# Performance work log

Hardware: AMD Instinct MI355X
Metric: run time of the kernel (lower is better)

The kernel has to match this reference:

```python
import jax, jax.numpy as jnp
import numpy as np
from jax import lax

B, CIN, COUT, H, W = 4, 256, 256, 64, 64
KH = KW = 3
K = KH * KW
GN_GROUPS = 32
EPS = 1e-5


def setup_inputs() -> dict:
    key = jax.random.key(0)
    ks = jax.random.split(key, 6)
    x = jax.random.normal(ks[0], (B, CIN, H, W), jnp.float32)
    # offset predictor conv: 3x3, 18 out channels, with bias (init small so offsets stay near 0)
    offset_w = jax.random.normal(ks[1], (2 * K, CIN, KH, KW), jnp.float32) * 0.01
    offset_b = jax.random.normal(ks[2], (2 * K,), jnp.float32) * 0.01
    # deformable conv weight (no bias), He-ish scale
    deform_w = jax.random.normal(ks[3], (COUT, CIN, KH, KW), jnp.float32) * (1.0 / np.sqrt(CIN * K))
    gn_gamma = jnp.ones((COUT,), jnp.float32)
    gn_beta = jnp.zeros((COUT,), jnp.float32)
    return {"x": x, "offset_w": offset_w, "offset_b": offset_b,
            "deform_w": deform_w, "gn_gamma": gn_gamma, "gn_beta": gn_beta}


def _deform_conv(x, offset, weight):
    """Deformable conv v1, stride=1, pad=1, dil=1, deformable_groups=1.
    x: [B,C,H,W]; offset: [B,2K,H,W] with (dy,dx) per kernel tap; weight: [O,C,3,3].
    """
    b, c, h, w = x.shape
    off = offset.reshape(b, K, 2, h, w)
    # base sampling grid per kernel tap: p = p0 - pad + k
    ky, kx = jnp.meshgrid(jnp.arange(KH), jnp.arange(KW), indexing="ij")
    base_y = (jnp.arange(h, dtype=jnp.float32) - 1.0)[None, :, None] + ky.reshape(K).astype(jnp.float32)[:, None, None]  # [K,H,1]
    base_x = (jnp.arange(w, dtype=jnp.float32) - 1.0)[None, None, :] + kx.reshape(K).astype(jnp.float32)[:, None, None]  # [K,1,W]
    py = base_y[None] + off[:, :, 0]  # [B,K,H,W]
    px = base_x[None] + off[:, :, 1]  # [B,K,H,W]

    y0 = jnp.floor(py)
    x0 = jnp.floor(px)
    ty = py - y0
    tx = px - x0
    y0 = y0.astype(jnp.int32)
    x0 = x0.astype(jnp.int32)

    x_hw = x.transpose(0, 2, 3, 1).reshape(b, h * w, c)  # [B,HW,C]

    def corner(yi, xi, wgt):
        valid = (yi >= 0) & (yi < h) & (xi >= 0) & (xi < w)
        yc = jnp.clip(yi, 0, h - 1)
        xc = jnp.clip(xi, 0, w - 1)
        idx = (yc * w + xc).reshape(b, K * h * w)
        v = jnp.take_along_axis(x_hw, idx[..., None], axis=1)  # [B,KHW,C]
        return v * (wgt * valid.astype(wgt.dtype)).reshape(b, K * h * w, 1)

    samp = (corner(y0, x0, (1 - ty) * (1 - tx))
            + corner(y0, x0 + 1, (1 - ty) * tx)
            + corner(y0 + 1, x0, ty * (1 - tx))
            + corner(y0 + 1, x0 + 1, ty * tx))  # [B,KHW,C]
    samp = samp.reshape(b, K, h, w, c)
    return jnp.einsum("bkhwc,ock->bohw", samp, weight.reshape(weight.shape[0], c, K))


def reference(x, offset_w, offset_b, deform_w, gn_gamma, gn_beta):
    # offset = conv3x3(x) + bias
    offset = lax.conv_general_dilated(
        x, offset_w, window_strides=(1, 1), padding=((1, 1), (1, 1)),
        dimension_numbers=("NCHW", "OIHW", "NCHW")) + offset_b[None, :, None, None]
    out = _deform_conv(x, offset, deform_w)
    # GroupNorm(32, COUT) + ReLU
    b, c, h, w = out.shape
    g = out.reshape(b, GN_GROUPS, (c // GN_GROUPS) * h * w)
    mu = g.mean(axis=2, keepdims=True)
    var = g.var(axis=2, keepdims=True)
    g = (g - mu) * lax.rsqrt(var + EPS)
    out = g.reshape(b, c, h, w) * gn_gamma[None, :, None, None] + gn_beta[None, :, None, None]
    return jax.nn.relu(out)
```

## Files before the change

kernel.cpp:

```cpp
#include <hip/hip_runtime.h>
#include <hip/hip_bf16.h>
#include <stdint.h>


typedef unsigned short u16;
typedef __bf16 bf16x8 __attribute__((ext_vector_type(8)));
typedef float f32x4_t __attribute__((ext_vector_type(4)));

#define HW 4096

__device__ __forceinline__ uint32_t f32_to_bf16_rne(float f) {
  uint32_t u = __builtin_bit_cast(uint32_t, f);
  return (u + 0x7FFFu + ((u >> 16) & 1u)) >> 16;
}
__device__ __forceinline__ float bf_lo(uint32_t u) {
  return __builtin_bit_cast(float, u << 16);
}
__device__ __forceinline__ float bf_hi(uint32_t u) {
  return __builtin_bit_cast(float, u & 0xFFFF0000u);
}
__device__ __forceinline__ uint32_t blend2(uint32_t a, uint32_t b, uint32_t c,
                                           uint32_t d, float4 mw) {
  float lo = mw.x * bf_lo(a) + mw.y * bf_lo(b) + mw.z * bf_lo(c) + mw.w * bf_lo(d);
  float hi = mw.x * bf_hi(a) + mw.y * bf_hi(b) + mw.z * bf_hi(c) + mw.w * bf_hi(d);
  return f32_to_bf16_rne(lo) | (f32_to_bf16_rne(hi) << 16);
}

__global__ __launch_bounds__(256) void k_pre(const float* __restrict__ x,
                                             const float* __restrict__ wsrc,
                                             const float* __restrict__ ow,
                                             u16* __restrict__ xt,
                                             u16* __restrict__ warr,
                                             u16* __restrict__ owm,
                                             float* __restrict__ part) {
  __shared__ float tile[64][65];
  int bid = blockIdx.x;
  int tid = threadIdx.x;
  int bz = bid >> 8;
  int c0 = ((bid >> 6) & 3) * 64;
  int p0 = (bid & 63) * 64;

  {
    int ch = tid >> 4;
    int q4 = (tid & 15) * 4;
#pragma unroll
    for (int r = 0; r < 4; r++) {
      int c = r * 16 + ch;
      float4 v = *(const float4*)&x[((size_t)(bz * 256 + c0 + c)) * HW + p0 + q4];
      tile[c][q4 + 0] = v.x;
      tile[c][q4 + 1] = v.y;
      tile[c][q4 + 2] = v.z;
      tile[c][q4 + 3] = v.w;
    }
  }
  __syncthreads();
  {
    int chunk = tid & 7;
    int pxr = tid >> 3;
#pragma unroll
    for (int it = 0; it < 2; it++) {
      int px = it * 32 + pxr;
      int cb = chunk * 8;
      uint4 u;
      u.x = f32_to_bf16_rne(tile[cb + 0][px]) | (f32_to_bf16_rne(tile[cb + 1][px]) << 16);
      u.y = f32_to_bf16_rne(tile[cb + 2][px]) | (f32_to_bf16_rne(tile[cb + 3][px]) << 16);
      u.z = f32_to_bf16_rne(tile[cb + 4][px]) | (f32_to_bf16_rne(tile[cb + 5][px]) << 16);
      u.w = f32_to_bf16_rne(tile[cb + 6][px]) | (f32_to_bf16_rne(tile[cb + 7][px]) << 16);
      *(uint4*)&xt[((size_t)(bz * HW + p0 + px)) * 256 + c0 + cb] = u;
    }
  }

#pragma unroll
  for (int k = 0; k < 3; k++) {
    int i = k * 256 + tid;
    if (i < 576) {
      int e = bid * 576 + i;
      int kk = e & 7, m = (e >> 3) & 255, g = (e >> 11) & 7, kc = e >> 14;
      int cin = (kc & 3) * 64 + g * 8 + kk;
      warr[e] = (u16)f32_to_bf16_rne(wsrc[m * 2304 + cin * 9 + (kc >> 2)]);
    }
  }
  if (tid < 72) {
    int e = bid * 72 + tid;
    int kk = e & 7, m = (e >> 3) & 31, g = (e >> 8) & 7, kc = e >> 11;
    int cin = (kc & 3) * 64 + g * 8 + kk;
    float v = (m < 18) ? ow[m * 2304 + cin * 9 + (kc >> 2)] : 0.f;
    owm[e] = (u16)f32_to_bf16_rne(v);
  }
  if (bid == 0 && tid < 256) part[tid] = 0.f;
}

__global__ __launch_bounds__(512, 4) void k_conv(
    const u16* __restrict__ xt, const u16* __restrict__ warr,
    const u16* __restrict__ owm, const float* __restrict__ ob,
    float* __restrict__ out, float* __restrict__ part) {
  __shared__ char smem[54272];
  u16* stage = (u16*)smem;
  float* off_part = (float*)(smem + 33792);
  int4* ci_s = (int4*)smem;
  float4* mw_s = (float4*)(smem + 4608);
  u16* b_s = (u16*)(smem + 9216);

  int tid = threadIdx.x;
  int lane = tid & 63;
  int wm = tid >> 6;
  int wk = (blockIdx.x & 7) * 64 + (blockIdx.x >> 3);
  int b = wk >> 7;
  int pt = wk & 127;
  int p0 = pt * 32;
  int yrow = p0 >> 6, xbase = p0 & 63;

  {
    u16* st = stage + wm * 2112;
    int q = lane & 15, pq = lane >> 4;
    int oct = lane & 7, pxs = lane >> 3;
    f32x4_t a2[2][2] = {};
#pragma unroll 1
    for (int kc = wm; kc < 36; kc += 8) {
      int tap = kc >> 2, cc = kc & 3;
      int ky = tap / 3, kx = tap % 3;
      int yy = yrow + ky - 1;
      bool vy = (yy >= 0) && (yy < 64);
#pragma unroll
      for (int i = 0; i < 4; i++) {
        int px = i * 8 + pxs;
        int xx2 = xbase + px + kx - 1;
        uint4 v = make_uint4(0u, 0u, 0u, 0u);
        if (vy && xx2 >= 0 && xx2 < 64)
          v = *(const uint4*)&xt[(b * HW + yy * 64 + xx2) * 256 + cc * 64 + oct * 8];
        *(uint4*)&st[oct * 264 + px * 8] = v;
      }
#pragma unroll
      for (int ks = 0; ks < 2; ks++) {
        int g = ks * 4 + pq;
        const u16* ab = owm + kc * 2048 + g * 256;
#pragma unroll
        for (int s = 0; s < 2; s++) {
          bf16x8 bfr = *(bf16x8*)&st[g * 264 + (s * 16 + q) * 8];
#pragma unroll
          for (int im = 0; im < 2; im++) {
            bf16x8 af = *(const bf16x8*)&ab[(im * 16 + q) * 8];
            a2[s][im] = __builtin_amdgcn_mfma_f32_16x16x32_bf16(af, bfr, a2[s][im], 0, 0, 0);
          }
        }
      }
    }
#pragma unroll
    for (int s = 0; s < 2; s++)
#pragma unroll
      for (int im = 0; im < 2; im++)
#pragma unroll
        for (int r = 0; r < 4; r++) {
          int oc = im * 16 + pq * 4 + r;
          if (oc < 18) off_part[(wm * 32 + s * 16 + q) * 20 + oc] = a2[s][im][r];
        }
  }
  __syncthreads();
  for (int it = tid; it < 288; it += 512) {
    int tap = it >> 5;
    int px = it & 31;
    float dy = ob[2 * tap], dx = ob[2 * tap + 1];
#pragma unroll
    for (int wv = 0; wv < 8; wv++) {
      dy += off_part[(wv * 32 + px) * 20 + 2 * tap];
      dx += off_part[(wv * 32 + px) * 20 + 2 * tap + 1];
    }
    int ky = tap / 3, kx = tap % 3;
    int p = p0 + px;
    int yq = p >> 6, xq = p & 63;
    float py = (float)(yq - 1 + ky) + dy;
    float pxx = (float)(xq - 1 + kx) + dx;
    float y0f = floorf(py), x0f = floorf(pxx);
    float ty = py - y0f, tx = pxx - x0f;
    int y0 = (int)y0f, x0 = (int)x0f;
    int y1 = y0 + 1, x1 = x0 + 1;
    float wy0 = 1.f - ty, wy1 = ty, wx0 = 1.f - tx, wx1 = tx;
    bool vy0 = (y0 >= 0) && (y0 < 64), vy1 = (y1 >= 0) && (y1 < 64);
    bool vx0 = (x0 >= 0) && (x0 < 64), vx1 = (x1 >= 0) && (x1 < 64);
    int cy0 = min(max(y0, 0), 63), cy1 = min(max(y1, 0), 63);
    int cx0 = min(max(x0, 0), 63), cx1 = min(max(x1, 0), 63);
    int base = b * HW;
    int4 ci;
    ci.x = (base + cy0 * 64 + cx0) * 256;
    ci.y = (base + cy0 * 64 + cx1) * 256;
    ci.z = (base + cy1 * 64 + cx0) * 256;
    ci.w = (base + cy1 * 64 + cx1) * 256;
    float4 mw;
    mw.x = wy0 * wx0 * ((vy0 && vx0) ? 1.f : 0.f);
    mw.y = wy0 * wx1 * ((vy0 && vx1) ? 1.f : 0.f);
    mw.z = wy1 * wx0 * ((vy1 && vx0) ? 1.f : 0.f);
    mw.w = wy1 * wx1 * ((vy1 && vx1) ? 1.f : 0.f);
    ci_s[it] = ci;
    mw_s[it] = mw;
  }
  __syncthreads();

  {
    int oct8 = tid & 15;
    int pxg = tid >> 4;
    int sub = pxg >> 4;
    int pxw = pxg & 15;
    int col = lane & 15;
    int pq = lane >> 4;
    int e0 = oct8 * 8;
    f32x4_t acc[2][2] = {};

    int4 ci = ci_s[pxg];
    float4 mw = mw_s[pxg];
    uint4 A0 = *(const uint4*)&xt[ci.x + e0];
    uint4 A1 = *(const uint4*)&xt[ci.y + e0];
    uint4 A2 = *(const uint4*)&xt[ci.z + e0];
    uint4 A3 = *(const uint4*)&xt[ci.w + e0];
    uint4 G0 = *(const uint4*)&xt[ci.x + 128 + e0];
    uint4 G1 = *(const uint4*)&xt[ci.y + 128 + e0];
    uint4 G2 = *(const uint4*)&xt[ci.z + 128 + e0];
    uint4 G3 = *(const uint4*)&xt[ci.w + 128 + e0];

#pragma unroll 1
    for (int dp = 0; dp < 9; dp++) {
      u16* bb = b_s + (dp & 1) * 8704;
      {
        uint4 u;
        u.x = blend2(A0.x, A1.x, A2.x, A3.x, mw);
        u.y = blend2(A0.y, A1.y, A2.y, A3.y, mw);
        u.z = blend2(A0.z, A1.z, A2.z, A3.z, mw);
        u.w = blend2(A0.w, A1.w, A2.w, A3.w, mw);
        *(uint4*)&bb[sub * 2176 + oct8 * 136 + pxw * 8] = u;
      }
      {
        uint4 v;
        v.x = blend2(G0.x, G1.x, G2.x, G3.x, mw);
        v.y = blend2(G0.y, G1.y, G2.y, G3.y, mw);
        v.z = blend2(G0.z, G1.z, G2.z, G3.z, mw);
        v.w = blend2(G0.w, G1.w, G2.w, G3.w, mw);
        *(uint4*)&bb[4352 + sub * 2176 + oct8 * 136 + pxw * 8] = v;
      }
      __syncthreads();
      if (dp < 8) {
        ci = ci_s[(dp + 1) * 32 + pxg];
        float4 mwn = mw_s[(dp + 1) * 32 + pxg];
        A0 = *(const uint4*)&xt[ci.x + e0];
        A1 = *(const uint4*)&xt[ci.y + e0];
        A2 = *(const uint4*)&xt[ci.z + e0];
        A3 = *(const uint4*)&xt[ci.w + e0];
        G0 = *(const uint4*)&xt[ci.x + 128 + e0];
        G1 = *(const uint4*)&xt[ci.y + 128 + e0];
        G2 = *(const uint4*)&xt[ci.z + 128 + e0];
        G3 = *(const uint4*)&xt[ci.w + 128 + e0];
        mw = mwn;
      }
      __builtin_amdgcn_s_setprio(1);
#pragma unroll
      for (int ks = 0; ks < 8; ks++) {
        int set = ks >> 2;
        int ro = (ks & 3) * 4 + pq;
        const u16* bp = bb + set * 4352 + ro * 136 + col * 8;
        bf16x8 bb0 = *(const bf16x8*)&bp[0];
        bf16x8 bb1 = *(const bf16x8*)&bp[2176];
        int kc = dp * 4 + (ks >> 1);
        int gg = (ks & 1) * 4 + pq;
        const u16* ab = warr + kc * 16384 + gg * 2048 + (wm * 32 + col) * 8;
#pragma unroll
        for (int im = 0; im < 2; im++) {
          bf16x8 af = *(const bf16x8*)&ab[im * 128];
          acc[0][im] = __builtin_amdgcn_mfma_f32_16x16x32_bf16(af, bb0, acc[0][im], 0, 0, 0);
          acc[1][im] = __builtin_amdgcn_mfma_f32_16x16x32_bf16(af, bb1, acc[1][im], 0, 0, 0);
        }
      }
      __builtin_amdgcn_s_setprio(0);
    }

#pragma unroll
    for (int im = 0; im < 2; im++) {
      float s = 0.f, ss = 0.f;
#pragma unroll
      for (int sb = 0; sb < 2; sb++) {
        int n = p0 + sb * 16 + col;
#pragma unroll
        for (int r = 0; r < 4; r++) {
          int m = wm * 32 + im * 16 + pq * 4 + r;
          float v = acc[sb][im][r];
          out[(b * 256 + m) * HW + n] = v;
          s += v;
          ss += v * v;
        }
      }
#pragma unroll
      for (int msk = 1; msk <= 16; msk <<= 1) {
        s += __shfl_xor(s, msk);
        ss += __shfl_xor(ss, msk);
      }
      if ((lane & 31) == 0) {
        int grp = wm * 4 + im * 2 + (lane >> 5);
        float* pp = part + (b * 32 + grp) * 2;
        atomicAdd(pp, s);
        atomicAdd(pp + 1, ss);
      }
    }
  }
}

__global__ __launch_bounds__(256) void k_gn_apply(float* __restrict__ out,
                                                  const float2* __restrict__ part,
                                                  const float* __restrict__ gamma,
                                                  const float* __restrict__ beta) {
  int base = blockIdx.x * 512 + threadIdx.x;
#pragma unroll
  for (int k = 0; k < 2; k++) {
    int gid = base + k * 256;
    int c = (gid >> 10) & 255;
    int bb = gid >> 18;
    float2 p = part[bb * 32 + (c >> 3)];
    float mu = p.x / 32768.f;
    float var = p.y / 32768.f - mu * mu;
    float rs = rsqrtf(var + 1e-5f);
    float ga = gamma[c] * rs;
    float be = beta[c] - mu * ga;
    float4 v = ((const float4*)out)[gid];
    v.x = fmaxf(v.x * ga + be, 0.f);
    v.y = fmaxf(v.y * ga + be, 0.f);
    v.z = fmaxf(v.z * ga + be, 0.f);
    v.w = fmaxf(v.w * ga + be, 0.f);
    ((float4*)out)[gid] = v;
  }
}

extern "C" void kernel_launch(void* const* d_in, const int* in_sizes, int n_in,
                              void* d_out, int out_size, void* d_ws, size_t ws_size,
                              hipStream_t stream) {
  const float* x = (const float*)d_in[0];
  const float* offset_w = (const float*)d_in[1];
  const float* offset_b = (const float*)d_in[2];
  const float* deform_w = (const float*)d_in[3];
  const float* gn_gamma = (const float*)d_in[4];
  const float* gn_beta = (const float*)d_in[5];
  float* out = (float*)d_out;
  char* ws = (char*)d_ws;

  u16* xt = (u16*)ws;
  u16* warr = (u16*)(ws + 8388608);
  u16* owm = (u16*)(ws + 9568256);
  float* part = (float*)(ws + 9715712);

  k_pre<<<dim3(1024), dim3(256), 0, stream>>>(x, deform_w, offset_w, xt, warr, owm, part);
  k_conv<<<dim3(512), dim3(512), 0, stream>>>(xt, warr, owm, offset_b, out, part);
  k_gn_apply<<<dim3(2048), dim3(256), 0, stream>>>(out, (const float2*)part, gn_gamma, gn_beta);
}
```

Measured before the change: 158.6 us.

## Fuse GroupNorm apply into conv kernel via per-batch grid barrier

Removes the separate GroupNorm/ReLU kernel. Each conv block now adds its partial statistics, signals a per-batch atomic counter, spins until all 128 blocks of that batch have arrived, then normalizes and applies ReLU to its accumulators before writing the output once. This drops the extra read and write of the full output tensor and one kernel launch. In exchange it relies on all 128 blocks of a batch being co-resident, since the spin barrier would deadlock otherwise, and blocks sit idle while they wait.

```diff
diff --git a/kernel.cpp b/kernel.cpp
--- a/kernel.cpp
+++ b/kernel.cpp
@@ -87,13 +87,17 @@
     float v = (m < 18) ? ow[m * 2304 + cin * 9 + (kc >> 2)] : 0.f;
     owm[e] = (u16)f32_to_bf16_rne(v);
   }
-  if (bid == 0 && tid < 256) part[tid] = 0.f;
+  if (bid == 0) {
+    if (tid < 256) part[tid] = 0.f;
+    if (tid < 4) ((int*)(part + 256))[tid] = 0;
+  }
 }
 
 __global__ __launch_bounds__(512, 4) void k_conv(
     const u16* __restrict__ xt, const u16* __restrict__ warr,
     const u16* __restrict__ owm, const float* __restrict__ ob,
-    float* __restrict__ out, float* __restrict__ part) {
+    const float* __restrict__ gamma, const float* __restrict__ beta,
+    float* __restrict__ out, float* __restrict__ part, int* __restrict__ cnt) {
   __shared__ char smem[54272];
   u16* stage = (u16*)smem;
   float* off_part = (float*)(smem + 33792);
@@ -195,15 +199,15 @@
   }
   __syncthreads();
 
+  int col = lane & 15;
+  int pq = lane >> 4;
+  f32x4_t acc[2][2] = {};
   {
     int oct8 = tid & 15;
     int pxg = tid >> 4;
     int sub = pxg >> 4;
     int pxw = pxg & 15;
-    int col = lane & 15;
-    int pq = lane >> 4;
     int e0 = oct8 * 8;
-    f32x4_t acc[2][2] = {};
 
     int4 ci = ci_s[pxg];
     float4 mw = mw_s[pxg];
@@ -269,59 +273,71 @@
       }
       __builtin_amdgcn_s_setprio(0);
     }
-
-#pragma unroll
-    for (int im = 0; im < 2; im++) {
-      float s = 0.f, ss = 0.f;
+  }
+
+#pragma unroll
+  for (int im = 0; im < 2; im++) {
+    float s = 0.f, ss = 0.f;
+#pragma unroll
+    for (int sb = 0; sb < 2; sb++)
+#pragma unroll
+      for (int r = 0; r < 4; r++) {
+        float v = acc[sb][im][r];
+        s += v;
+        ss += v * v;
+      }
+#pragma unroll
+    for (int msk = 1; msk <= 16; msk <<= 1) {
+      s += __shfl_xor(s, msk);
+      ss += __shfl_xor(ss, msk);
+    }
+    if ((lane & 31) == 0) {
+      int grp = wm * 4 + im * 2 + (lane >> 5);
+      float* pp = part + (b * 32 + grp) * 2;
+      atomicAdd(pp, s);
+      atomicAdd(pp + 1, ss);
+    }
+  }
+
+  __threadfence();
+  __syncthreads();
+  if (tid == 0) {
+    __hip_atomic_fetch_add(&cnt[b], 1, __ATOMIC_ACQ_REL, __HIP_MEMORY_SCOPE_AGENT);
+    while (__hip_atomic_load(&cnt[b], __ATOMIC_ACQUIRE, __HIP_MEMORY_SCOPE_AGENT) < 128) {
+      __builtin_amdgcn_s_sleep(2);
+    }
+  }
+  __syncthreads();
+
+  float* gmu = (float*)smem;
+  float* grs = (float*)(smem + 128);
+  if (tid < 32) {
+    float s = __hip_atomic_load(&part[(b * 32 + tid) * 2], __ATOMIC_RELAXED,
+                                __HIP_MEMORY_SCOPE_AGENT);
+    float ss = __hip_atomic_load(&part[(b * 32 + tid) * 2 + 1], __ATOMIC_RELAXED,
+                                 __HIP_MEMORY_SCOPE_AGENT);
+    float mu = s * (1.f / 32768.f);
+    float var = ss * (1.f / 32768.f) - mu * mu;
+    gmu[tid] = mu;
+    grs[tid] = rsqrtf(var + 1e-5f);
+  }
+  __syncthreads();
+
+#pragma unroll
+  for (int im = 0; im < 2; im++) {
+    int grp = wm * 4 + im * 2 + (lane >> 5);
+    float mu = gmu[grp], rs = grs[grp];
+#pragma unroll
+    for (int r = 0; r < 4; r++) {
+      int m = wm * 32 + im * 16 + pq * 4 + r;
+      float ga = gamma[m] * rs;
+      float be = beta[m] - mu * ga;
 #pragma unroll
       for (int sb = 0; sb < 2; sb++) {
         int n = p0 + sb * 16 + col;
-#pragma unroll
-        for (int r = 0; r < 4; r++) {
-          int m = wm * 32 + im * 16 + pq * 4 + r;
-          float v = acc[sb][im][r];
-          out[(b * 256 + m) * HW + n] = v;
-          s += v;
-          ss += v * v;
-        }
-      }
-#pragma unroll
-      for (int msk = 1; msk <= 16; msk <<= 1) {
-        s += __shfl_xor(s, msk);
-        ss += __shfl_xor(ss, msk);
-      }
-      if ((lane & 31) == 0) {
-        int grp = wm * 4 + im * 2 + (lane >> 5);
-        float* pp = part + (b * 32 + grp) * 2;
-        atomicAdd(pp, s);
-        atomicAdd(pp + 1, ss);
-      }
-    }
-  }
-}
-
-__global__ __launch_bounds__(256) void k_gn_apply(float* __restrict__ out,
-                                                  const float2* __restrict__ part,
-                                                  const float* __restrict__ gamma,
-                                                  const float* __restrict__ beta) {
-  int base = blockIdx.x * 512 + threadIdx.x;
-#pragma unroll
-  for (int k = 0; k < 2; k++) {
-    int gid = base + k * 256;
-    int c = (gid >> 10) & 255;
-    int bb = gid >> 18;
-    float2 p = part[bb * 32 + (c >> 3)];
-    float mu = p.x / 32768.f;
-    float var = p.y / 32768.f - mu * mu;
-    float rs = rsqrtf(var + 1e-5f);
-    float ga = gamma[c] * rs;
-    float be = beta[c] - mu * ga;
-    float4 v = ((const float4*)out)[gid];
-    v.x = fmaxf(v.x * ga + be, 0.f);
-    v.y = fmaxf(v.y * ga + be, 0.f);
-    v.z = fmaxf(v.z * ga + be, 0.f);
-    v.w = fmaxf(v.w * ga + be, 0.f);
-    ((float4*)out)[gid] = v;
+        out[(b * 256 + m) * HW + n] = fmaxf(acc[sb][im][r] * ga + be, 0.f);
+      }
+    }
   }
 }
 
@@ -341,8 +357,9 @@
   u16* warr = (u16*)(ws + 8388608);
   u16* owm = (u16*)(ws + 9568256);
   float* part = (float*)(ws + 9715712);
+  int* cnt = (int*)(ws + 9715712 + 1024);
 
   k_pre<<<dim3(1024), dim3(256), 0, stream>>>(x, deform_w, offset_w, xt, warr, owm, part);
-  k_conv<<<dim3(512), dim3(512), 0, stream>>>(xt, warr, owm, offset_b, out, part);
-  k_gn_apply<<<dim3(2048), dim3(256), 0, stream>>>(out, (const float2*)part, gn_gamma, gn_beta);
-}
+  k_conv<<<dim3(512), dim3(512), 0, stream>>>(xt, warr, owm, offset_b, gn_gamma,
+                                              gn_beta, out, part, cnt);
+}
```

New measurement: 215.3 us. +35.8%, slower.

## Halve conv block pixel tile to 16 with 4 waves each covering 64 channels

Applied to the files above, without the earlier changes.

The fused deformable-conv kernel now handles 16 pixels per block with 256 threads instead of 32 pixels with 512 threads, doubling the grid to 1024 blocks. Each wave now computes 64 output channels against one 16-pixel B fragment, so four MFMAs share each B load. The offset-predictor conv is redistributed over 4 waves by tap. Shared memory drops from about 54KB to 22KB, which should allow more resident blocks and spread the work more evenly. The cost is that each weight fragment is reused across fewer pixels, so global weight reads per output roughly double, and per-block setup overhead is repeated more often.

```diff
diff --git a/kernel.cpp b/kernel.cpp
--- a/kernel.cpp
+++ b/kernel.cpp
@@ -90,80 +90,78 @@
   if (bid == 0 && tid < 256) part[tid] = 0.f;
 }
 
-__global__ __launch_bounds__(512, 4) void k_conv(
+__global__ __launch_bounds__(256, 4) void k_conv(
     const u16* __restrict__ xt, const u16* __restrict__ warr,
     const u16* __restrict__ owm, const float* __restrict__ ob,
     float* __restrict__ out, float* __restrict__ part) {
-  __shared__ char smem[54272];
+  __shared__ char smem[22016];
   u16* stage = (u16*)smem;
-  float* off_part = (float*)(smem + 33792);
+  float* off_part = (float*)(smem + 8704);
   int4* ci_s = (int4*)smem;
-  float4* mw_s = (float4*)(smem + 4608);
-  u16* b_s = (u16*)(smem + 9216);
+  float4* mw_s = (float4*)(smem + 2304);
+  u16* b_s = (u16*)(smem + 4608);
 
   int tid = threadIdx.x;
   int lane = tid & 63;
   int wm = tid >> 6;
-  int wk = (blockIdx.x & 7) * 64 + (blockIdx.x >> 3);
-  int b = wk >> 7;
-  int pt = wk & 127;
-  int p0 = pt * 32;
+  int wk = (blockIdx.x & 7) * 128 + (blockIdx.x >> 3);
+  int b = wk >> 8;
+  int pt = wk & 255;
+  int p0 = pt * 16;
   int yrow = p0 >> 6, xbase = p0 & 63;
 
   {
-    u16* st = stage + wm * 2112;
+    u16* st = stage + wm * 1088;
     int q = lane & 15, pq = lane >> 4;
     int oct = lane & 7, pxs = lane >> 3;
-    f32x4_t a2[2][2] = {};
+    f32x4_t a2[2] = {};
 #pragma unroll 1
-    for (int kc = wm; kc < 36; kc += 8) {
-      int tap = kc >> 2, cc = kc & 3;
+    for (int tap = wm; tap < 9; tap += 4) {
       int ky = tap / 3, kx = tap % 3;
       int yy = yrow + ky - 1;
       bool vy = (yy >= 0) && (yy < 64);
 #pragma unroll
-      for (int i = 0; i < 4; i++) {
-        int px = i * 8 + pxs;
-        int xx2 = xbase + px + kx - 1;
-        uint4 v = make_uint4(0u, 0u, 0u, 0u);
-        if (vy && xx2 >= 0 && xx2 < 64)
-          v = *(const uint4*)&xt[(b * HW + yy * 64 + xx2) * 256 + cc * 64 + oct * 8];
-        *(uint4*)&st[oct * 264 + px * 8] = v;
-      }
-#pragma unroll
-      for (int ks = 0; ks < 2; ks++) {
-        int g = ks * 4 + pq;
-        const u16* ab = owm + kc * 2048 + g * 256;
-#pragma unroll
-        for (int s = 0; s < 2; s++) {
-          bf16x8 bfr = *(bf16x8*)&st[g * 264 + (s * 16 + q) * 8];
+      for (int cc = 0; cc < 4; cc++) {
+        int kc = tap * 4 + cc;
+#pragma unroll
+        for (int i = 0; i < 2; i++) {
+          int px = i * 8 + pxs;
+          int xx2 = xbase + px + kx - 1;
+          uint4 v = make_uint4(0u, 0u, 0u, 0u);
+          if (vy && xx2 >= 0 && xx2 < 64)
+            v = *(const uint4*)&xt[(b * HW + yy * 64 + xx2) * 256 + cc * 64 + oct * 8];
+          *(uint4*)&st[oct * 136 + px * 8] = v;
+        }
+#pragma unroll
+        for (int ks = 0; ks < 2; ks++) {
+          int g = ks * 4 + pq;
+          const u16* ab = owm + kc * 2048 + g * 256;
+          bf16x8 bfr = *(bf16x8*)&st[g * 136 + q * 8];
 #pragma unroll
           for (int im = 0; im < 2; im++) {
             bf16x8 af = *(const bf16x8*)&ab[(im * 16 + q) * 8];
-            a2[s][im] = __builtin_amdgcn_mfma_f32_16x16x32_bf16(af, bfr, a2[s][im], 0, 0, 0);
+            a2[im] = __builtin_amdgcn_mfma_f32_16x16x32_bf16(af, bfr, a2[im], 0, 0, 0);
           }
         }
       }
     }
 #pragma unroll
-    for (int s = 0; s < 2; s++)
-#pragma unroll
-      for (int im = 0; im < 2; im++)
-#pragma unroll
-        for (int r = 0; r < 4; r++) {
-          int oc = im * 16 + pq * 4 + r;
-          if (oc < 18) off_part[(wm * 32 + s * 16 + q) * 20 + oc] = a2[s][im][r];
-        }
+    for (int im = 0; im < 2; im++)
+#pragma unroll
+      for (int r = 0; r < 4; r++) {
+        int oc = im * 16 + pq * 4 + r;
+        if (oc < 18) off_part[(wm * 16 + q) * 20 + oc] = a2[im][r];
+      }
   }
   __syncthreads();
-  for (int it = tid; it < 288; it += 512) {
-    int tap = it >> 5;
-    int px = it & 31;
+  if (tid < 144) {
+    int tap = tid >> 4;
+    int px = tid & 15;
     float dy = ob[2 * tap], dx = ob[2 * tap + 1];
 #pragma unroll
-    for (int wv = 0; wv < 8; wv++) {
-      dy += off_part[(wv * 32 + px) * 20 + 2 * tap];
-      dx += off_part[(wv * 32 + px) * 20 + 2 * tap + 1];
+    for (int wv = 0; wv < 4; wv++) {
+      dy += off_part[(wv * 16 + px) * 20 + 2 * tap];
+      dx += off_part[(wv * 16 + px) * 20 + 2 * tap + 1];
     }
     int ky = tap / 3, kx = tap % 3;
     int p = p0 + px;
@@ -190,20 +188,18 @@
     mw.y = wy0 * wx1 * ((vy0 && vx1) ? 1.f : 0.f);
     mw.z = wy1 * wx0 * ((vy1 && vx0) ? 1.f : 0.f);
     mw.w = wy1 * wx1 * ((vy1 && vx1) ? 1.f : 0.f);
-    ci_s[it] = ci;
-    mw_s[it] = mw;
+    ci_s[tid] = ci;
+    mw_s[tid] = mw;
   }
   __syncthreads();
 
+  int col = lane & 15;
+  int pq = lane >> 4;
   {
     int oct8 = tid & 15;
     int pxg = tid >> 4;
-    int sub = pxg >> 4;
-    int pxw = pxg & 15;
-    int col = lane & 15;
-    int pq = lane >> 4;
     int e0 = oct8 * 8;
-    f32x4_t acc[2][2] = {};
+    f32x4_t acc[4] = {};
 
     int4 ci = ci_s[pxg];
     float4 mw = mw_s[pxg];
@@ -218,14 +214,14 @@
 
 #pragma unroll 1
     for (int dp = 0; dp < 9; dp++) {
-      u16* bb = b_s + (dp & 1) * 8704;
+      u16* bb = b_s + (dp & 1) * 4352;
       {
         uint4 u;
         u.x = blend2(A0.x, A1.x, A2.x, A3.x, mw);
         u.y = blend2(A0.y, A1.y, A2.y, A3.y, mw);
         u.z = blend2(A0.z, A1.z, A2.z, A3.z, mw);
         u.w = blend2(A0.w, A1.w, A2.w, A3.w, mw);
-        *(uint4*)&bb[sub * 2176 + oct8 * 136 + pxw * 8] = u;
+        *(uint4*)&bb[oct8 * 136 + pxg * 8] = u;
       }
       {
         uint4 v;
@@ -233,12 +229,12 @@
         v.y = blend2(G0.y, G1.y, G2.y, G3.y, mw);
         v.z = blend2(G0.z, G1.z, G2.z, G3.z, mw);
         v.w = blend2(G0.w, G1.w, G2.w, G3.w, mw);
-        *(uint4*)&bb[4352 + sub * 2176 + oct8 * 136 + pxw * 8] = v;
+        *(uint4*)&bb[2176 + oct8 * 136 + pxg * 8] = v;
       }
       __syncthreads();
       if (dp < 8) {
-        ci = ci_s[(dp + 1) * 32 + pxg];
-        float4 mwn = mw_s[(dp + 1) * 32 + pxg];
+        ci = ci_s[(dp + 1) * 16 + pxg];
+        float4 mwn = mw_s[(dp + 1) * 16 + pxg];
         A0 = *(const uint4*)&xt[ci.x + e0];
         A1 = *(const uint4*)&xt[ci.y + e0];
         A2 = *(const uint4*)&xt[ci.z + e0];
@@ -254,36 +250,30 @@
       for (int ks = 0; ks < 8; ks++) {
         int set = ks >> 2;
         int ro = (ks & 3) * 4 + pq;
-        const u16* bp = bb + set * 4352 + ro * 136 + col * 8;
-        bf16x8 bb0 = *(const bf16x8*)&bp[0];
-        bf16x8 bb1 = *(const bf16x8*)&bp[2176];
+        bf16x8 bbv = *(const bf16x8*)&bb[set * 2176 + ro * 136 + col * 8];
         int kc = dp * 4 + (ks >> 1);
         int gg = (ks & 1) * 4 + pq;
-        const u16* ab = warr + kc * 16384 + gg * 2048 + (wm * 32 + col) * 8;
-#pragma unroll
-        for (int im = 0; im < 2; im++) {
+        const u16* ab = warr + kc * 16384 + gg * 2048 + (wm * 64 + col) * 8;
+#pragma unroll
+        for (int im = 0; im < 4; im++) {
           bf16x8 af = *(const bf16x8*)&ab[im * 128];
-          acc[0][im] = __builtin_amdgcn_mfma_f32_16x16x32_bf16(af, bb0, acc[0][im], 0, 0, 0);
-          acc[1][im] = __builtin_amdgcn_mfma_f32_16x16x32_bf16(af, bb1, acc[1][im], 0, 0, 0);
+          acc[im] = __builtin_amdgcn_mfma_f32_16x16x32_bf16(af, bbv, acc[im], 0, 0, 0);
         }
       }
       __builtin_amdgcn_s_setprio(0);
     }
 
 #pragma unroll
-    for (int im = 0; im < 2; im++) {
+    for (int im = 0; im < 4; im++) {
       float s = 0.f, ss = 0.f;
-#pragma unroll
-      for (int sb = 0; sb < 2; sb++) {
-        int n = p0 + sb * 16 + col;
-#pragma unroll
-        for (int r = 0; r < 4; r++) {
-          int m = wm * 32 + im * 16 + pq * 4 + r;
-          float v = acc[sb][im][r];
-          out[(b * 256 + m) * HW + n] = v;
-          s += v;
-          ss += v * v;
-        }
+      int n = p0 + col;
+#pragma unroll
+      for (int r = 0; r < 4; r++) {
+        int m = wm * 64 + im * 16 + pq * 4 + r;
+        float v = acc[im][r];
+        out[(b * 256 + m) * HW + n] = v;
+        s += v;
+        ss += v * v;
       }
 #pragma unroll
       for (int msk = 1; msk <= 16; msk <<= 1) {
@@ -291,7 +281,7 @@
         ss += __shfl_xor(ss, msk);
       }
       if ((lane & 31) == 0) {
-        int grp = wm * 4 + im * 2 + (lane >> 5);
+        int grp = wm * 8 + im * 2 + (lane >> 5);
         float* pp = part + (b * 32 + grp) * 2;
         atomicAdd(pp, s);
         atomicAdd(pp + 1, ss);
@@ -343,6 +333,6 @@
   float* part = (float*)(ws + 9715712);
 
   k_pre<<<dim3(1024), dim3(256), 0, stream>>>(x, deform_w, offset_w, xt, warr, owm, part);
-  k_conv<<<dim3(512), dim3(512), 0, stream>>>(xt, warr, owm, offset_b, out, part);
+  k_conv<<<dim3(1024), dim3(256), 0, stream>>>(xt, warr, owm, offset_b, out, part);
   k_gn_apply<<<dim3(2048), dim3(256), 0, stream>>>(out, (const float2*)part, gn_gamma, gn_beta);
 }
```

New measurement: 194.6 us. 1.23x slower.
